# Kernel optimization log

Hardware: AMD Instinct MI355X
Metric: run time of the kernel (lower is better)

## Reference

```python
import jax, jax.numpy as jnp
import numpy as np

RADIUS = 0.05      # outer ball-query radius
MIN_RADIUS = 0.02  # inner exclusion radius


def setup_inputs() -> dict:
    key = jax.random.key(0)
    k1, k2 = jax.random.split(key)
    # raw layout is [B, C, N, 1] as consumed by forward's squeeze(-1).permute(0,2,1)
    xyz = jax.random.uniform(k1, (4, 3, 4096, 1), dtype=jnp.float32)      # coords in unit cube
    points = jax.random.normal(k2, (4, 64, 4096, 1), dtype=jnp.float32)   # per-point features
    return {"xyz": xyz, "points": points}


def _pairwise_sqdist(x):
    # x: [B, N, 3] -> [B, N, N] squared euclidean distances
    sq = jnp.sum(x * x, axis=-1)  # [B, N]
    return sq[:, :, None] + sq[:, None, :] - 2.0 * jnp.einsum('bnc,bmc->bnm', x, x)


def reference(xyz, points):
    # [B, C, N, 1] -> [B, N, C]
    _xyz = jnp.transpose(xyz[..., 0], (0, 2, 1))       # [B, N, 3]
    _points = jnp.transpose(points[..., 0], (0, 2, 1))  # [B, N, D]
    B, N, C = _xyz.shape

    # downsample_query_ball: ball-query neighbor counts in annulus (min_radius, radius),
    # keep the N//2 densest points
    d2 = _pairwise_sqdist(_xyz)                              # [B, N, N]
    nbr_cnt = jnp.sum(((d2 < RADIUS ** 2) & (d2 > MIN_RADIUS ** 2)).astype(jnp.int32), axis=-1)
    _, idx = jax.lax.top_k(nbr_cnt, N // 2)                  # [B, N//2]

    # index_points: gather along the point axis
    new_xyz = jnp.take_along_axis(_xyz, idx[..., None], axis=1)        # [B, N//2, 3]
    new_points = jnp.take_along_axis(_points, idx[..., None], axis=1)  # [B, N//2, D]
    return new_xyz, new_points
```

## Files before the change

### kernel.cpp

```cpp
#include <hip/hip_runtime.h>


#define BN 4
#define NPTS 4096
#define ND 64
#define KSEL 2048
#define R2 0.0025f
#define M2 0.0004f

#define IPT 4
#define ITILES 4
#define JC 32
#define JCH 128

__global__ __launch_bounds__(256) void count_part_kernel(
        const float* __restrict__ xyz, int* __restrict__ part) {
    __shared__ float4 sj[JCH];
    const int jc = blockIdx.x & (JC - 1);
    const int it = (blockIdx.x >> 5) & (ITILES - 1);
    const int b  = blockIdx.x >> 7;
    const float* base = xyz + (size_t)b * 3 * NPTS;

    if (threadIdx.x < JCH) {
        int j = jc * JCH + threadIdx.x;
        float x = base[j], y = base[NPTS + j], z = base[2 * NPTS + j];
        float sq = __fadd_rn(__fadd_rn(__fmul_rn(x, x), __fmul_rn(y, y)),
                             __fmul_rn(z, z));
        sj[threadIdx.x] = make_float4(x, y, z, sq);
    }
    const int ibase = it * 1024 + threadIdx.x;
    float4 mi[IPT];
    #pragma unroll
    for (int k = 0; k < IPT; ++k) {
        int i = ibase + k * 256;
        float x = base[i], y = base[NPTS + i], z = base[2 * NPTS + i];
        float sq = __fadd_rn(__fadd_rn(__fmul_rn(x, x), __fmul_rn(y, y)),
                             __fmul_rn(z, z));
        mi[k] = make_float4(x, y, z, sq);
    }
    __syncthreads();

    int cnt[IPT] = {0, 0, 0, 0};
    #pragma unroll 4
    for (int j = 0; j < JCH; ++j) {
        float4 p = sj[j];
        #pragma unroll
        for (int k = 0; k < IPT; ++k) {
            float dot = __fadd_rn(__fadd_rn(__fmul_rn(mi[k].x, p.x),
                                            __fmul_rn(mi[k].y, p.y)),
                                  __fmul_rn(mi[k].z, p.z));
            float d2 = __fsub_rn(__fadd_rn(mi[k].w, p.w), __fmul_rn(2.0f, dot));
            cnt[k] += (d2 < R2 && d2 > M2) ? 1 : 0;
        }
    }
    int* pp = part + (size_t)((b * ITILES + it) * JC + jc) * 1024;
    #pragma unroll
    for (int k = 0; k < IPT; ++k) pp[threadIdx.x + k * 256] = cnt[k];
}

__global__ __launch_bounds__(256) void key_kernel(
        const int* __restrict__ part, int* __restrict__ key) {
    int tid = blockIdx.x * 256 + threadIdx.x;
    int b = tid >> 12, i = tid & (NPTS - 1);
    int it = i >> 10, local = i & 1023;
    const int* pp = part + (size_t)(b * ITILES + it) * JC * 1024 + local;
    int c = 0;
    #pragma unroll
    for (int jc = 0; jc < JC; ++jc) c += pp[jc * 1024];
    key[tid] = (c << 12) | (NPTS - 1 - i);
}

__global__ __launch_bounds__(256) void rank_gather_kernel(
        const float* __restrict__ xyz, const float* __restrict__ points,
        const int* __restrict__ key, float* __restrict__ out) {
    __shared__ int skey[NPTS];
    __shared__ int spr[4][64];
    __shared__ int srank[64];
    const int b     = blockIdx.x >> 6;
    const int tbase = (blockIdx.x & 63) * 64;
    const int* kb = key + b * NPTS;
    for (int idx = threadIdx.x; idx < NPTS; idx += 256) skey[idx] = kb[idx];
    __syncthreads();

    const int ii = threadIdx.x & 63;
    const int q  = threadIdx.x >> 6;
    const int ki = skey[tbase + ii];
    int r = 0;
    #pragma unroll 8
    for (int j = q * 1024; j < q * 1024 + 1024; ++j)
        r += (skey[j] > ki) ? 1 : 0;
    spr[q][ii] = r;
    __syncthreads();

    if (threadIdx.x < 64) {
        int rank = spr[0][threadIdx.x] + spr[1][threadIdx.x] +
                   spr[2][threadIdx.x] + spr[3][threadIdx.x];
        srank[threadIdx.x] = rank;
        int i = tbase + threadIdx.x;
        if (rank < KSEL) {
            const float* xb = xyz + (size_t)b * 3 * NPTS;
            float* o = out + ((size_t)b * KSEL + rank) * 3;
            o[0] = xb[i]; o[1] = xb[NPTS + i]; o[2] = xb[2 * NPTS + i];
        }
    }
    __syncthreads();

    const int rank = srank[ii];
    float* ofeat = out + (size_t)BN * KSEL * 3;
    for (int c = q; c < ND; c += 4) {
        float v = points[((size_t)b * ND + c) * NPTS + tbase + ii];
        if (rank < KSEL) ofeat[((size_t)b * KSEL + rank) * ND + c] = v;
    }
}

extern "C" void kernel_launch(void* const* d_in, const int* in_sizes, int n_in,
                              void* d_out, int out_size, void* d_ws, size_t ws_size,
                              hipStream_t stream) {
    const float* xyz    = (const float*)d_in[0];
    const float* points = (const float*)d_in[1];
    float* out = (float*)d_out;

    char* ws = (char*)d_ws;
    int* part = (int*)ws;
    int* key  = (int*)(ws + 2 * 1024 * 1024);

    count_part_kernel<<<BN * ITILES * JC, 256, 0, stream>>>(xyz, part);
    key_kernel<<<BN * NPTS / 256, 256, 0, stream>>>(part, key);
    rank_gather_kernel<<<BN * 64, 256, 0, stream>>>(xyz, points, key, out);
}
```

Measured before the change: 91.43 us.

## Fuse count, key and rank-gather stages into one cooperative kernel with grid syncs

Merges the three launches into a single cooperative kernel of 512 blocks, separated by grid-wide barriers, to remove launch gaps between small kernels. The key reduction now uses 8 threads per point with shuffle reductions, and the rank stage reads keys as int4 with 32 points per block across 8 quarter-slices. The cost is two grid syncs, plus a requirement that all 512 blocks be co-resident for the cooperative launch; shared memory is reused between stages.

```diff
diff --git a/kernel.cpp b/kernel.cpp
--- a/kernel.cpp
+++ b/kernel.cpp
@@ -1,4 +1,7 @@
 #include <hip/hip_runtime.h>
+#include <hip/hip_cooperative_groups.h>
+
+namespace cg = cooperative_groups;
 
 
 #define BN 4
@@ -12,104 +15,140 @@
 #define ITILES 4
 #define JC 32
 #define JCH 128
+#define GRID (BN * ITILES * JC)
 
-__global__ __launch_bounds__(256) void count_part_kernel(
-        const float* __restrict__ xyz, int* __restrict__ part) {
-    __shared__ float4 sj[JCH];
-    const int jc = blockIdx.x & (JC - 1);
-    const int it = (blockIdx.x >> 5) & (ITILES - 1);
-    const int b  = blockIdx.x >> 7;
-    const float* base = xyz + (size_t)b * 3 * NPTS;
+__global__ __launch_bounds__(256, 2) void pool_fused_kernel(
+        const float* __restrict__ xyz, const float* __restrict__ points,
+        int* __restrict__ part, int* __restrict__ key,
+        float* __restrict__ out) {
+    cg::grid_group grid = cg::this_grid();
 
-    if (threadIdx.x < JCH) {
-        int j = jc * JCH + threadIdx.x;
-        float x = base[j], y = base[NPTS + j], z = base[2 * NPTS + j];
-        float sq = __fadd_rn(__fadd_rn(__fmul_rn(x, x), __fmul_rn(y, y)),
-                             __fmul_rn(z, z));
-        sj[threadIdx.x] = make_float4(x, y, z, sq);
+    __shared__ alignas(16) int skey[NPTS];
+    __shared__ int spr[8][32];
+    __shared__ int srank[32];
+
+    const int blk = blockIdx.x;
+    const int tid = threadIdx.x;
+
+    {
+        float4* sj = (float4*)skey;
+        const int jc = blk & (JC - 1);
+        const int it = (blk >> 5) & (ITILES - 1);
+        const int b  = blk >> 7;
+        const float* base = xyz + (size_t)b * 3 * NPTS;
+
+        if (tid < JCH) {
+            int j = jc * JCH + tid;
+            float x = base[j], y = base[NPTS + j], z = base[2 * NPTS + j];
+            float sq = __fadd_rn(__fadd_rn(__fmul_rn(x, x), __fmul_rn(y, y)),
+                                 __fmul_rn(z, z));
+            sj[tid] = make_float4(x, y, z, sq);
+        }
+        const int ibase = it * 1024 + tid;
+        float4 mi[IPT];
+        #pragma unroll
+        for (int k = 0; k < IPT; ++k) {
+            int i = ibase + k * 256;
+            float x = base[i], y = base[NPTS + i], z = base[2 * NPTS + i];
+            float sq = __fadd_rn(__fadd_rn(__fmul_rn(x, x), __fmul_rn(y, y)),
+                                 __fmul_rn(z, z));
+            mi[k] = make_float4(x, y, z, sq);
+        }
+        __syncthreads();
+
+        int cnt[IPT] = {0, 0, 0, 0};
+        #pragma unroll 4
+        for (int j = 0; j < JCH; ++j) {
+            float4 p = sj[j];
+            #pragma unroll
+            for (int k = 0; k < IPT; ++k) {
+                float dot = __fadd_rn(__fadd_rn(__fmul_rn(mi[k].x, p.x),
+                                                __fmul_rn(mi[k].y, p.y)),
+                                      __fmul_rn(mi[k].z, p.z));
+                float d2 = __fsub_rn(__fadd_rn(mi[k].w, p.w),
+                                     __fmul_rn(2.0f, dot));
+                cnt[k] += (d2 < R2 && d2 > M2) ? 1 : 0;
+            }
+        }
+        int* pp = part + (size_t)((b * ITILES + it) * JC + jc) * 1024;
+        #pragma unroll
+        for (int k = 0; k < IPT; ++k) pp[tid + k * 256] = cnt[k];
     }
-    const int ibase = it * 1024 + threadIdx.x;
-    float4 mi[IPT];
-    #pragma unroll
-    for (int k = 0; k < IPT; ++k) {
-        int i = ibase + k * 256;
-        float x = base[i], y = base[NPTS + i], z = base[2 * NPTS + i];
-        float sq = __fadd_rn(__fadd_rn(__fmul_rn(x, x), __fmul_rn(y, y)),
-                             __fmul_rn(z, z));
-        mi[k] = make_float4(x, y, z, sq);
+
+    grid.sync();
+
+    {
+        const int p    = blk * 32 + (tid >> 3);
+        const int tid8 = tid & 7;
+        const int b2    = p >> 12;
+        const int i2    = p & (NPTS - 1);
+        const int it2   = i2 >> 10;
+        const int local = i2 & 1023;
+        const int* pb = part + (size_t)(b2 * ITILES + it2) * JC * 1024 + local;
+        int c = 0;
+        #pragma unroll
+        for (int u = 0; u < 4; ++u) c += pb[(tid8 * 4 + u) * 1024];
+        c += __shfl_down(c, 4, 8);
+        c += __shfl_down(c, 2, 8);
+        c += __shfl_down(c, 1, 8);
+        if (tid8 == 0) key[p] = (c << 12) | (NPTS - 1 - i2);
+    }
+
+    grid.sync();
+
+    const int b3    = blk >> 7;
+    const int tbase = (blk & 127) * 32;
+    {
+        const int4* kg = (const int4*)(key + (size_t)b3 * NPTS);
+        int4* sk4 = (int4*)skey;
+        #pragma unroll
+        for (int idx = tid; idx < NPTS / 4; idx += 256) sk4[idx] = kg[idx];
     }
     __syncthreads();
 
-    int cnt[IPT] = {0, 0, 0, 0};
-    #pragma unroll 4
-    for (int j = 0; j < JCH; ++j) {
-        float4 p = sj[j];
-        #pragma unroll
-        for (int k = 0; k < IPT; ++k) {
-            float dot = __fadd_rn(__fadd_rn(__fmul_rn(mi[k].x, p.x),
-                                            __fmul_rn(mi[k].y, p.y)),
-                                  __fmul_rn(mi[k].z, p.z));
-            float d2 = __fsub_rn(__fadd_rn(mi[k].w, p.w), __fmul_rn(2.0f, dot));
-            cnt[k] += (d2 < R2 && d2 > M2) ? 1 : 0;
+    {
+        const int pi = tid & 31;
+        const int q  = tid >> 5;
+        const int ki = skey[tbase + pi];
+        const int4* sk4 = (const int4*)skey;
+        int r = 0;
+        #pragma unroll 4
+        for (int jj = q * 128; jj < q * 128 + 128; ++jj) {
+            int4 v = sk4[jj];
+            r += (v.x > ki) ? 1 : 0;
+            r += (v.y > ki) ? 1 : 0;
+            r += (v.z > ki) ? 1 : 0;
+            r += (v.w > ki) ? 1 : 0;
         }
+        spr[q][pi] = r;
     }
-    int* pp = part + (size_t)((b * ITILES + it) * JC + jc) * 1024;
-    #pragma unroll
-    for (int k = 0; k < IPT; ++k) pp[threadIdx.x + k * 256] = cnt[k];
-}
-
-__global__ __launch_bounds__(256) void key_kernel(
-        const int* __restrict__ part, int* __restrict__ key) {
-    int tid = blockIdx.x * 256 + threadIdx.x;
-    int b = tid >> 12, i = tid & (NPTS - 1);
-    int it = i >> 10, local = i & 1023;
-    const int* pp = part + (size_t)(b * ITILES + it) * JC * 1024 + local;
-    int c = 0;
-    #pragma unroll
-    for (int jc = 0; jc < JC; ++jc) c += pp[jc * 1024];
-    key[tid] = (c << 12) | (NPTS - 1 - i);
-}
-
-__global__ __launch_bounds__(256) void rank_gather_kernel(
-        const float* __restrict__ xyz, const float* __restrict__ points,
-        const int* __restrict__ key, float* __restrict__ out) {
-    __shared__ int skey[NPTS];
-    __shared__ int spr[4][64];
-    __shared__ int srank[64];
-    const int b     = blockIdx.x >> 6;
-    const int tbase = (blockIdx.x & 63) * 64;
-    const int* kb = key + b * NPTS;
-    for (int idx = threadIdx.x; idx < NPTS; idx += 256) skey[idx] = kb[idx];
     __syncthreads();
 
-    const int ii = threadIdx.x & 63;
-    const int q  = threadIdx.x >> 6;
-    const int ki = skey[tbase + ii];
-    int r = 0;
-    #pragma unroll 8
-    for (int j = q * 1024; j < q * 1024 + 1024; ++j)
-        r += (skey[j] > ki) ? 1 : 0;
-    spr[q][ii] = r;
-    __syncthreads();
-
-    if (threadIdx.x < 64) {
-        int rank = spr[0][threadIdx.x] + spr[1][threadIdx.x] +
-                   spr[2][threadIdx.x] + spr[3][threadIdx.x];
-        srank[threadIdx.x] = rank;
-        int i = tbase + threadIdx.x;
+    if (tid < 32) {
+        int rank = 0;
+        #pragma unroll
+        for (int q = 0; q < 8; ++q) rank += spr[q][tid];
+        srank[tid] = rank;
+        const int i = tbase + tid;
         if (rank < KSEL) {
-            const float* xb = xyz + (size_t)b * 3 * NPTS;
-            float* o = out + ((size_t)b * KSEL + rank) * 3;
+            const float* xb = xyz + (size_t)b3 * 3 * NPTS;
+            float* o = out + ((size_t)b3 * KSEL + rank) * 3;
             o[0] = xb[i]; o[1] = xb[NPTS + i]; o[2] = xb[2 * NPTS + i];
         }
     }
     __syncthreads();
 
-    const int rank = srank[ii];
-    float* ofeat = out + (size_t)BN * KSEL * 3;
-    for (int c = q; c < ND; c += 4) {
-        float v = points[((size_t)b * ND + c) * NPTS + tbase + ii];
-        if (rank < KSEL) ofeat[((size_t)b * KSEL + rank) * ND + c] = v;
+    {
+        const int pt = tid & 31;
+        const int cw = tid >> 5;
+        const int rank = srank[pt];
+        float* ofeat = out + (size_t)BN * KSEL * 3;
+        #pragma unroll
+        for (int r8 = 0; r8 < 8; ++r8) {
+            int c = cw + 8 * r8;
+            float v = points[((size_t)b3 * ND + c) * NPTS + tbase + pt];
+            if (rank < KSEL) ofeat[((size_t)b3 * KSEL + rank) * ND + c] = v;
+        }
     }
 }
 
@@ -124,7 +163,8 @@
     int* part = (int*)ws;
     int* key  = (int*)(ws + 2 * 1024 * 1024);
 
-    count_part_kernel<<<BN * ITILES * JC, 256, 0, stream>>>(xyz, part);
-    key_kernel<<<BN * NPTS / 256, 256, 0, stream>>>(part, key);
-    rank_gather_kernel<<<BN * 64, 256, 0, stream>>>(xyz, points, key, out);
+    void* args[] = {(void*)&xyz, (void*)&points, (void*)&part,
+                    (void*)&key, (void*)&out};
+    hipLaunchCooperativeKernel((const void*)pool_fused_kernel,
+                               dim3(GRID), dim3(256), args, 0, stream);
 }
```

Measured after the change: 178.6 us. 95.3% more time.

## Fuse key computation into rank-gather kernel and vectorize rank counting

Applied to the files above, without the earlier changes.

Removes the separate key kernel: each rank/gather block now sums the per-chunk partial neighbour counts itself using int4 loads and builds the sort keys directly in shared memory. The rank comparison loop reads keys as int4 to cut LDS instructions, and the feature gather loop is fully unrolled. This saves a kernel launch and a global round trip for keys, but every block redundantly re-reads the whole per-batch partial-count buffer, multiplying cache traffic.

```diff
diff --git a/kernel.cpp b/kernel.cpp
--- a/kernel.cpp
+++ b/kernel.cpp
@@ -58,45 +58,65 @@
     for (int k = 0; k < IPT; ++k) pp[threadIdx.x + k * 256] = cnt[k];
 }
 
-__global__ __launch_bounds__(256) void key_kernel(
-        const int* __restrict__ part, int* __restrict__ key) {
-    int tid = blockIdx.x * 256 + threadIdx.x;
-    int b = tid >> 12, i = tid & (NPTS - 1);
-    int it = i >> 10, local = i & 1023;
-    const int* pp = part + (size_t)(b * ITILES + it) * JC * 1024 + local;
-    int c = 0;
-    #pragma unroll
-    for (int jc = 0; jc < JC; ++jc) c += pp[jc * 1024];
-    key[tid] = (c << 12) | (NPTS - 1 - i);
-}
-
 __global__ __launch_bounds__(256) void rank_gather_kernel(
         const float* __restrict__ xyz, const float* __restrict__ points,
-        const int* __restrict__ key, float* __restrict__ out) {
-    __shared__ int skey[NPTS];
+        const int* __restrict__ part, float* __restrict__ out) {
+    __shared__ alignas(16) int skey[NPTS];
     __shared__ int spr[4][64];
     __shared__ int srank[64];
     const int b     = blockIdx.x >> 6;
     const int tbase = (blockIdx.x & 63) * 64;
-    const int* kb = key + b * NPTS;
-    for (int idx = threadIdx.x; idx < NPTS; idx += 256) skey[idx] = kb[idx];
+    const int tid   = threadIdx.x;
+
+    {
+        int4* sk4 = (int4*)skey;
+        const int* pbase = part + (size_t)b * ITILES * JC * 1024;
+        #pragma unroll
+        for (int gg = 0; gg < 4; ++gg) {
+            const int g    = tid + gg * 256;
+            const int it   = g >> 8;
+            const int loc4 = (g & 255) * 4;
+            const int4* pp =
+                (const int4*)(pbase + (size_t)it * JC * 1024 + loc4);
+            int4 s = make_int4(0, 0, 0, 0);
+            #pragma unroll 8
+            for (int jc = 0; jc < JC; ++jc) {
+                int4 v = pp[jc * 256];
+                s.x += v.x; s.y += v.y; s.z += v.z; s.w += v.w;
+            }
+            const int i0 = it * 1024 + loc4;
+            int4 kv;
+            kv.x = (s.x << 12) | (NPTS - 1 - (i0 + 0));
+            kv.y = (s.y << 12) | (NPTS - 1 - (i0 + 1));
+            kv.z = (s.z << 12) | (NPTS - 1 - (i0 + 2));
+            kv.w = (s.w << 12) | (NPTS - 1 - (i0 + 3));
+            sk4[g] = kv;
+        }
+    }
     __syncthreads();
 
-    const int ii = threadIdx.x & 63;
-    const int q  = threadIdx.x >> 6;
-    const int ki = skey[tbase + ii];
-    int r = 0;
-    #pragma unroll 8
-    for (int j = q * 1024; j < q * 1024 + 1024; ++j)
-        r += (skey[j] > ki) ? 1 : 0;
-    spr[q][ii] = r;
+    {
+        const int pi = tid & 63;
+        const int q  = tid >> 6;
+        const int ki = skey[tbase + pi];
+        const int4* sk4 = (const int4*)skey;
+        int r = 0;
+        #pragma unroll 8
+        for (int jj = q * 256; jj < q * 256 + 256; ++jj) {
+            int4 v = sk4[jj];
+            r += (v.x > ki) ? 1 : 0;
+            r += (v.y > ki) ? 1 : 0;
+            r += (v.z > ki) ? 1 : 0;
+            r += (v.w > ki) ? 1 : 0;
+        }
+        spr[q][pi] = r;
+    }
     __syncthreads();
 
-    if (threadIdx.x < 64) {
-        int rank = spr[0][threadIdx.x] + spr[1][threadIdx.x] +
-                   spr[2][threadIdx.x] + spr[3][threadIdx.x];
-        srank[threadIdx.x] = rank;
-        int i = tbase + threadIdx.x;
+    if (tid < 64) {
+        const int rank = spr[0][tid] + spr[1][tid] + spr[2][tid] + spr[3][tid];
+        srank[tid] = rank;
+        const int i = tbase + tid;
         if (rank < KSEL) {
             const float* xb = xyz + (size_t)b * 3 * NPTS;
             float* o = out + ((size_t)b * KSEL + rank) * 3;
@@ -105,11 +125,17 @@
     }
     __syncthreads();
 
-    const int rank = srank[ii];
-    float* ofeat = out + (size_t)BN * KSEL * 3;
-    for (int c = q; c < ND; c += 4) {
-        float v = points[((size_t)b * ND + c) * NPTS + tbase + ii];
-        if (rank < KSEL) ofeat[((size_t)b * KSEL + rank) * ND + c] = v;
+    {
+        const int ii   = tid & 63;
+        const int q    = tid >> 6;
+        const int rank = srank[ii];
+        float* ofeat = out + (size_t)BN * KSEL * 3;
+        #pragma unroll
+        for (int r16 = 0; r16 < 16; ++r16) {
+            const int c = q + 4 * r16;
+            float v = points[((size_t)b * ND + c) * NPTS + tbase + ii];
+            if (rank < KSEL) ofeat[((size_t)b * KSEL + rank) * ND + c] = v;
+        }
     }
 }
 
@@ -119,12 +145,8 @@
     const float* xyz    = (const float*)d_in[0];
     const float* points = (const float*)d_in[1];
     float* out = (float*)d_out;
-
-    char* ws = (char*)d_ws;
-    int* part = (int*)ws;
-    int* key  = (int*)(ws + 2 * 1024 * 1024);
+    int* part = (int*)d_ws;
 
     count_part_kernel<<<BN * ITILES * JC, 256, 0, stream>>>(xyz, part);
-    key_kernel<<<BN * NPTS / 256, 256, 0, stream>>>(part, key);
-    rank_gather_kernel<<<BN * 64, 256, 0, stream>>>(xyz, points, key, out);
+    rank_gather_kernel<<<BN * 64, 256, 0, stream>>>(xyz, points, part, out);
 }
```

Result: no change. 90.38 us (-1.1%).
